# Optimization experiments

Hardware: AMD Instinct MI355X
Metric: run time of the kernel (lower is better)

## Reference

```python
import jax, jax.numpy as jnp
import numpy as np

XY, Z, NT = 10, 5, 10000
S = XY * XY * Z  # 500 states
NEG = np.float32(-1e9)  # finite stand-in for log(0); exp(NEG - m) == 0 in fp32


def _build_log_transitions(rng):
    # Reproduce initialize_transitions(): per-row softmax over the 7-neighbor
    # stencil [(0,0,0),(1,0,0),(-1,0,0),(0,1,0),(0,-1,0),(0,0,1),(0,0,2)],
    # zeros (=> log -inf) elsewhere. Vectorized construction.
    s = np.arange(S)
    z, r = np.divmod(s, XY * XY)
    y, x = np.divmod(r, XY)
    coords = np.stack([x, y, z], -1)                      # [S,3]
    offsets = np.array([[0,0,0],[1,0,0],[-1,0,0],[0,1,0],[0,-1,0],[0,0,1],[0,0,2]])
    nb = coords[:, None, :] + offsets[None, :, :]         # [S,7,3]
    valid = ((nb[..., 0] >= 0) & (nb[..., 0] < XY) &
             (nb[..., 1] >= 0) & (nb[..., 1] < XY) &
             (nb[..., 2] >= 0) & (nb[..., 2] < Z))
    dest = nb[..., 0] + XY * (nb[..., 1] + XY * nb[..., 2])  # [S,7]
    mask = np.zeros((S, S), bool)
    rows = np.broadcast_to(s[:, None], (S, 7))
    mask[rows[valid], dest[valid]] = True
    logits = rng.standard_normal((S, S)).astype(np.float32)
    logits = np.where(mask, logits, NEG)
    m = logits.max(-1, keepdims=True)
    lse = m + np.log(np.exp(logits - m).sum(-1, keepdims=True))
    logT = np.where(mask, (logits - lse).astype(np.float32), NEG)
    return jnp.asarray(logT)


def setup_inputs() -> dict:
    key = jax.random.key(0)
    k1, k2, k3 = jax.random.split(key, 3)
    rng = np.random.default_rng(0)
    B, T, L = 32, 40, 20
    log_priors = jax.nn.log_softmax(jax.random.normal(k1, (S,), dtype=jnp.float32))
    log_emissions = jax.nn.log_softmax(
        jax.random.normal(k2, (S, NT), dtype=jnp.float32), axis=-1)
    log_transitions = _build_log_transitions(rng)
    stories_tensor = jax.random.randint(k3, (B, T, L), 0, NT)
    return {
        "log_priors": log_priors,
        "log_transitions": log_transitions,
        "log_emissions": log_emissions,
        "stories_tensor": stories_tensor,
        "story_length": T,
    }


def reference(log_priors, log_transitions, log_emissions, stories_tensor, story_length):
    # Emission log-probs per (story, time): sum token log-probs over sentence.
    # log_emissions.T: [NT, S]; stories_tensor: [B, T, L] -> em: [B, T, S]
    em = jnp.take(log_emissions.T, stories_tensor, axis=0).sum(axis=2)
    alpha0 = em[:, 0] + log_priors  # [B, S]

    def step(alpha, em_t):
        # broadcast-add then logsumexp over source state (last axis)
        new = em_t + jax.nn.logsumexp(
            log_transitions[None, :, :] + alpha[:, None, :], axis=-1)
        return new, new

    _, rest = jax.lax.scan(step, alpha0, jnp.swapaxes(em[:, 1:], 0, 1))
    return jnp.concatenate([alpha0[None], rest], axis=0)  # [T, B, S]
```

## Files before the change

kernel.cpp:

```cpp
#include <hip/hip_runtime.h>

#define S   500
#define B   32
#define T   40
#define L   20
#define NT  10000
#define NEG (-1e9f)

__global__ __launch_bounds__(256) void emission_kernel(
    const float* __restrict__ logE, const int* __restrict__ stories,
    float* __restrict__ out)
{
    __shared__ float row[NT];
    const int s   = blockIdx.x;
    const int tid = threadIdx.x;

    const float4* src = (const float4*)(logE + (size_t)s * NT);
    float4* dst = (float4*)row;
    for (int i = tid; i < NT / 4; i += 256) dst[i] = src[i];
    __syncthreads();

    for (int p = tid; p < B * T; p += 256) {
        const int* tk = stories + p * L;
        float acc = 0.f;
        #pragma unroll
        for (int l = 0; l < L; ++l) acc += row[tk[l]];
        const int b = p / T, t = p % T;
        out[((size_t)t * B + b) * S + s] = acc;
    }
}

__global__ __launch_bounds__(512) void forward_kernel(
    const float* __restrict__ priors, const float* __restrict__ logT,
    float* __restrict__ out)
{
    __shared__ float alpha[2][512];
    const int s = threadIdx.x;
    const int b = blockIdx.x;
    const bool act = (s < S);

    float tv[7];
    int   dd[7];
    if (act) {
        const int x = s % 10, y = (s / 10) % 10, z = s / 100;
        const float* rowT = logT + (size_t)s * S;
        dd[0] = s;                          tv[0] = rowT[s];
        dd[1] = (x + 1 < 10) ? s + 1   : s; tv[1] = (x + 1 < 10) ? rowT[s + 1]   : NEG;
        dd[2] = (x - 1 >= 0) ? s - 1   : s; tv[2] = (x - 1 >= 0) ? rowT[s - 1]   : NEG;
        dd[3] = (y + 1 < 10) ? s + 10  : s; tv[3] = (y + 1 < 10) ? rowT[s + 10]  : NEG;
        dd[4] = (y - 1 >= 0) ? s - 10  : s; tv[4] = (y - 1 >= 0) ? rowT[s - 10]  : NEG;
        dd[5] = (z + 1 < 5)  ? s + 100 : s; tv[5] = (z + 1 < 5)  ? rowT[s + 100] : NEG;
        dd[6] = (z + 2 < 5)  ? s + 200 : s; tv[6] = (z + 2 < 5)  ? rowT[s + 200] : NEG;
    }

    const size_t base = (size_t)b * S + s;
    float a0 = 0.f;
    if (act) {
        a0 = out[base] + priors[s];
        out[base] = a0;
    }
    alpha[0][s] = a0;

    float em_next = 0.f;
    if (act) em_next = out[(size_t)B * S + base];
    __syncthreads();

    for (int t = 1; t < T; ++t) {
        const int cur = t & 1, prev = cur ^ 1;
        const float em_t = em_next;
        if (act && t + 1 < T) em_next = out[(size_t)(t + 1) * B * S + base];

        float a = 0.f;
        if (act) {
            const float v0 = tv[0] + alpha[prev][dd[0]];
            const float v1 = tv[1] + alpha[prev][dd[1]];
            const float v2 = tv[2] + alpha[prev][dd[2]];
            const float v3 = tv[3] + alpha[prev][dd[3]];
            const float v4 = tv[4] + alpha[prev][dd[4]];
            const float v5 = tv[5] + alpha[prev][dd[5]];
            const float v6 = tv[6] + alpha[prev][dd[6]];
            float m = fmaxf(fmaxf(fmaxf(v0, v1), fmaxf(v2, v3)),
                            fmaxf(fmaxf(v4, v5), v6));
            float sum = __expf(v0 - m) + __expf(v1 - m) + __expf(v2 - m) +
                        __expf(v3 - m) + __expf(v4 - m) + __expf(v5 - m) +
                        __expf(v6 - m);
            a = em_t + m + __logf(sum);
            out[(size_t)t * B * S + base] = a;
        }
        alpha[cur][s] = a;
        __syncthreads();
    }
}

extern "C" void kernel_launch(void* const* d_in, const int* in_sizes, int n_in,
                              void* d_out, int out_size, void* d_ws, size_t ws_size,
                              hipStream_t stream) {
    const float* priors  = (const float*)d_in[0];
    const float* logT    = (const float*)d_in[1];
    const float* logE    = (const float*)d_in[2];
    const int*   stories = (const int*)d_in[3];
    float* out = (float*)d_out;

    emission_kernel<<<S, 256, 0, stream>>>(logE, stories, out);
    forward_kernel<<<B, 512, 0, stream>>>(priors, logT, out);
}
```

Before: 108.2 us.

## Process two states per emission block, fold priors, keep self alpha in register

The emission kernel now stages two emission rows per block in shared memory, so each story's token indices are read once and reused for two states. Tokens are loaded as int4 and results stored as float2. The prior addition moves from the forward kernel into the emission kernel at t=0. The forward recursion keeps a state's own previous alpha in a register instead of reading it from shared memory. The cost is 80KB of shared memory per block and half as many emission blocks, which lowers occupancy and parallelism.

```diff
diff --git a/kernel.cpp b/kernel.cpp
--- a/kernel.cpp
+++ b/kernel.cpp
@@ -7,32 +7,40 @@
 #define NT  10000
 #define NEG (-1e9f)
 
-__global__ __launch_bounds__(256) void emission_kernel(
+__global__ __launch_bounds__(512) void emission_kernel(
     const float* __restrict__ logE, const int* __restrict__ stories,
-    float* __restrict__ out)
+    const float* __restrict__ priors, float* __restrict__ out)
 {
-    __shared__ float row[NT];
-    const int s   = blockIdx.x;
+    __shared__ float row0[NT];
+    __shared__ float row1[NT];
+    const int s0  = blockIdx.x * 2;
     const int tid = threadIdx.x;
 
-    const float4* src = (const float4*)(logE + (size_t)s * NT);
-    float4* dst = (float4*)row;
-    for (int i = tid; i < NT / 4; i += 256) dst[i] = src[i];
+    const float4* a  = (const float4*)(logE + (size_t)s0 * NT);
+    const float4* bsrc = (const float4*)(logE + (size_t)(s0 + 1) * NT);
+    float4* d0 = (float4*)row0;
+    float4* d1 = (float4*)row1;
+    for (int i = tid; i < NT / 4; i += 512) { d0[i] = a[i]; d1[i] = bsrc[i]; }
     __syncthreads();
 
-    for (int p = tid; p < B * T; p += 256) {
-        const int* tk = stories + p * L;
-        float acc = 0.f;
+    const float p0 = priors[s0], p1 = priors[s0 + 1];
+    for (int p = tid; p < B * T; p += 512) {
+        const int4* tk = (const int4*)(stories + p * L);
+        float acc0 = 0.f, acc1 = 0.f;
         #pragma unroll
-        for (int l = 0; l < L; ++l) acc += row[tk[l]];
+        for (int q = 0; q < L / 4; ++q) {
+            const int4 v = tk[q];
+            acc0 += row0[v.x] + row0[v.y] + row0[v.z] + row0[v.w];
+            acc1 += row1[v.x] + row1[v.y] + row1[v.z] + row1[v.w];
+        }
         const int b = p / T, t = p % T;
-        out[((size_t)t * B + b) * S + s] = acc;
+        if (t == 0) { acc0 += p0; acc1 += p1; }
+        *(float2*)(out + ((size_t)t * B + b) * S + s0) = make_float2(acc0, acc1);
     }
 }
 
 __global__ __launch_bounds__(512) void forward_kernel(
-    const float* __restrict__ priors, const float* __restrict__ logT,
-    float* __restrict__ out)
+    const float* __restrict__ logT, float* __restrict__ out)
 {
     __shared__ float alpha[2][512];
     const int s = threadIdx.x;
@@ -44,7 +52,7 @@
     if (act) {
         const int x = s % 10, y = (s / 10) % 10, z = s / 100;
         const float* rowT = logT + (size_t)s * S;
-        dd[0] = s;                          tv[0] = rowT[s];
+        tv[0] = rowT[s];
         dd[1] = (x + 1 < 10) ? s + 1   : s; tv[1] = (x + 1 < 10) ? rowT[s + 1]   : NEG;
         dd[2] = (x - 1 >= 0) ? s - 1   : s; tv[2] = (x - 1 >= 0) ? rowT[s - 1]   : NEG;
         dd[3] = (y + 1 < 10) ? s + 10  : s; tv[3] = (y + 1 < 10) ? rowT[s + 10]  : NEG;
@@ -54,12 +62,9 @@
     }
 
     const size_t base = (size_t)b * S + s;
-    float a0 = 0.f;
-    if (act) {
-        a0 = out[base] + priors[s];
-        out[base] = a0;
-    }
-    alpha[0][s] = a0;
+    float self = 0.f;
+    if (act) self = out[base];
+    alpha[0][s] = self;
 
     float em_next = 0.f;
     if (act) em_next = out[(size_t)B * S + base];
@@ -72,7 +77,7 @@
 
         float a = 0.f;
         if (act) {
-            const float v0 = tv[0] + alpha[prev][dd[0]];
+            const float v0 = tv[0] + self;
             const float v1 = tv[1] + alpha[prev][dd[1]];
             const float v2 = tv[2] + alpha[prev][dd[2]];
             const float v3 = tv[3] + alpha[prev][dd[3]];
@@ -88,6 +93,7 @@
             out[(size_t)t * B * S + base] = a;
         }
         alpha[cur][s] = a;
+        self = a;
         __syncthreads();
     }
 }
@@ -101,6 +107,6 @@
     const int*   stories = (const int*)d_in[3];
     float* out = (float*)d_out;
 
-    emission_kernel<<<S, 256, 0, stream>>>(logE, stories, out);
-    forward_kernel<<<B, 512, 0, stream>>>(priors, logT, out);
+    emission_kernel<<<S / 2, 512, 0, stream>>>(logE, stories, priors, out);
+    forward_kernel<<<B, 512, 0, stream>>>(logT, out);
 }
```

After: 99.77 us. 7.8% less time.
